# Kernel tuning notes

Measured on AMD Instinct MI355X. Metric: run time of the kernel, lower is better.

Reference implementation:

```python
import jax, jax.numpy as jnp
import numpy as np

B, T_ENC, IN, H, SEQ_OUT = 1024, 50, 99, 2112, 25


def _lstm_cell(x, h, c, W_ih, b_ih, W_hh, b_hh):
    # gates: [B, 4H], torch LSTMCell gate order is i, f, g, o
    gates = x @ W_ih.T + b_ih + h @ W_hh.T + b_hh
    i, f, g, o = jnp.split(gates, 4, axis=-1)
    c_new = jax.nn.sigmoid(f) * c + jax.nn.sigmoid(i) * jnp.tanh(g)
    h_new = jax.nn.sigmoid(o) * jnp.tanh(c_new)
    return h_new, c_new


def setup_inputs() -> dict:
    key = jax.random.key(0)
    ks = jax.random.split(key, 14)
    s = 0.04
    return {
        "hidden_states": jax.random.normal(ks[0], (B, T_ENC, H), jnp.float32),
        "cell_states": jax.random.normal(ks[1], (B, T_ENC, H), jnp.float32),
        "global_t_state": jax.random.normal(ks[2], (B, H), jnp.float32),
        "p": jax.random.normal(ks[3], (B, 1, IN), jnp.float32),
        "W_ih0": jax.random.normal(ks[4], (4 * H, IN), jnp.float32) * s,
        "b_ih0": jax.random.normal(ks[5], (4 * H,), jnp.float32) * s,
        "W_hh0": jax.random.normal(ks[6], (4 * H, H), jnp.float32) * s,
        "b_hh0": jax.random.normal(ks[7], (4 * H,), jnp.float32) * s,
        "W_ih1": jax.random.normal(ks[8], (4 * H, H), jnp.float32) * s,
        "b_ih1": jax.random.normal(ks[9], (4 * H,), jnp.float32) * s,
        "W_hh1": jax.random.normal(ks[10], (4 * H, H), jnp.float32) * s,
        "b_hh1": jax.random.normal(ks[11], (4 * H,), jnp.float32) * s,
        "W_out": jax.random.normal(ks[12], (H, IN), jnp.float32) * s,
        "b_out": jax.random.normal(ks[13], (IN,), jnp.float32) * s,
    }


def reference(hidden_states, cell_states, global_t_state, p,
              W_ih0, b_ih0, W_hh0, b_hh0,
              W_ih1, b_ih1, W_hh1, b_hh1,
              W_out, b_out):
    # initial states: layer 0 uses mean over encoder hidden states,
    # layer 1 uses mean over [global_t_state ; hidden_states]
    h0 = hidden_states.mean(axis=1)                                   # [B, H]
    h1 = jnp.concatenate((global_t_state[:, None, :], hidden_states), axis=1).mean(axis=1)
    c0 = cell_states.mean(axis=1)
    c1 = c0
    pre0 = p[:, 0, :]                                                 # seed input [B, IN]

    def step(carry, _):
        h0, c0, h1, c1, prev = carry
        h0n, c0n = _lstm_cell(prev, h0, c0, W_ih0, b_ih0, W_hh0, b_hh0)
        h1n, c1n = _lstm_cell(h0n, h1, c1, W_ih1, b_ih1, W_hh1, b_hh1)
        pre = h1n @ W_out + b_out + prev                              # residual on cell-0 input
        return (h0n, c0n, h1n, c1n, pre), pre

    _, pres = jax.lax.scan(step, (h0, c0, h1, c1, pre0), None, length=SEQ_OUT)
    return pres.transpose(1, 0, 2)                                    # [B, SEQ_OUT, IN]
```

## Files before the change

kernel.cpp:

```cpp
#include <hip/hip_runtime.h>

#define B_    1024
#define H_    2112
#define FH    8448
#define IN_   99
#define TENC  50
#define SEQ   25
#define K0    2240
#define K1    4224
#define LDX0  2240
#define LDX1  4224

typedef __bf16 bf16;
typedef __bf16 bf16x8 __attribute__((ext_vector_type(8)));
typedef __bf16 bf16x4 __attribute__((ext_vector_type(4)));
typedef float  f32x4  __attribute__((ext_vector_type(4)));

__device__ __forceinline__ void gload_lds16(const void* g, void* l) {
  __builtin_amdgcn_global_load_lds(
      (const __attribute__((address_space(1))) void*)g,
      (__attribute__((address_space(3))) void*)l, 16, 0, 0);
}

__device__ __forceinline__ float sigf(float x) { return 1.f / (1.f + __expf(-x)); }
__device__ __forceinline__ float tanhfast(float x) { return 1.f - 2.f / (__expf(2.f * x) + 1.f); }

__global__ __launch_bounds__(128, 3)
void lstm_gemm_cell(const bf16* __restrict__ X, int lda, int K,
                    const bf16* __restrict__ W,
                    const float* __restrict__ bsum,
                    float* __restrict__ Cst,
                    bf16* __restrict__ d1, int ld1,
                    bf16* __restrict__ d2, int ld2)
{
  __shared__ __align__(16) bf16 As[128 * 64];
  __shared__ __align__(16) bf16 Bs[64 * 64];

  const int cpx = gridDim.x >> 3;
  const int vid = (blockIdx.x & 7) * cpx + (blockIdx.x >> 3);
  const int hc0 = (vid >> 3) * 16;
  const int m0  = (vid & 7) * 128;

  const int tid  = threadIdx.x;
  const int srow = tid >> 3;
  const int scol = ((tid & 7) ^ (srow & 7)) * 8;

  const bf16* Ab = X + (size_t)(m0 + srow) * lda + scol;
  const bf16* Bb = W + (size_t)(hc0 + srow) * K + scol;

  const int lane = tid & 63;
  const int w    = tid >> 6;
  const int lr   = lane & 15, lq = lane >> 4;
  const int xs   = lr & 7;
  const int cof0 = (lq ^ xs) * 8;
  const int cof1 = ((4 + lq) ^ xs) * 8;

  f32x4 acc[4][4];
#pragma unroll
  for (int a = 0; a < 4; ++a)
#pragma unroll
    for (int b = 0; b < 4; ++b) acc[a][b] = (f32x4){0.f, 0.f, 0.f, 0.f};

  const int KT = K >> 6;
  for (int kt = 0; kt < KT; ++kt) {
    const int ko = kt * 64;
#pragma unroll
    for (int it = 0; it < 8; ++it)
      gload_lds16(Ab + (size_t)it * 16 * lda + ko, &As[it * 1024 + tid * 8]);
#pragma unroll
    for (int it = 0; it < 4; ++it)
      gload_lds16(Bb + (size_t)it * H_ * K + ko, &Bs[it * 1024 + tid * 8]);
    __syncthreads();

    bf16x8 af[4][2], bfr[4][2];
#pragma unroll
    for (int mi = 0; mi < 4; ++mi) {
      const int r = (w * 64 + mi * 16 + lr) * 64;
      af[mi][0] = *(const bf16x8*)&As[r + cof0];
      af[mi][1] = *(const bf16x8*)&As[r + cof1];
    }
#pragma unroll
    for (int nf = 0; nf < 4; ++nf) {
      const int r = (nf * 16 + lr) * 64;
      bfr[nf][0] = *(const bf16x8*)&Bs[r + cof0];
      bfr[nf][1] = *(const bf16x8*)&Bs[r + cof1];
    }
#pragma unroll
    for (int mi = 0; mi < 4; ++mi)
#pragma unroll
      for (int nf = 0; nf < 4; ++nf)
#pragma unroll
        for (int kc = 0; kc < 2; ++kc)
          acc[mi][nf] = __builtin_amdgcn_mfma_f32_16x16x32_bf16(
              af[mi][kc], bfr[nf][kc], acc[mi][nf], 0, 0, 0);
    __syncthreads();
  }

  const int hc = hc0 + lr;
  const float bi  = bsum[hc];
  const float bff = bsum[H_ + hc];
  const float bg  = bsum[2 * H_ + hc];
  const float bo  = bsum[3 * H_ + hc];

#pragma unroll
  for (int mi = 0; mi < 4; ++mi) {
#pragma unroll
    for (int r = 0; r < 4; ++r) {
      const int m = m0 + w * 64 + mi * 16 + lq * 4 + r;
      const float gi = acc[mi][0][r] + bi;
      const float gf = acc[mi][1][r] + bff;
      const float gg = acc[mi][2][r] + bg;
      const float go = acc[mi][3][r] + bo;
      const size_t ci = (size_t)m * H_ + hc;
      const float c_old = Cst[ci];
      const float cn = sigf(gf) * c_old + sigf(gi) * tanhfast(gg);
      const float hn = sigf(go) * tanhfast(cn);
      Cst[ci] = cn;
      const bf16 hb = (bf16)hn;
      d1[(size_t)m * ld1 + hc] = hb;
      if (d2) d2[(size_t)m * ld2 + hc] = hb;
    }
  }
}

__global__ __launch_bounds__(256, 1)
void out_gemm(const bf16* __restrict__ Hin,
              const bf16* __restrict__ Wo,
              const float* __restrict__ b_out,
              float* __restrict__ prev,
              bf16* __restrict__ X0n,
              float* __restrict__ out, int t)
{
  __shared__ float red[4][8][112];
  const int tid = threadIdx.x;
  const int m0 = blockIdx.x * 8;
  const int lane = tid & 63, wv = tid >> 6;
  const int lr = lane & 15, lq = lane >> 4, lk = lq * 8;

  f32x4 acc[7];
#pragma unroll
  for (int b = 0; b < 7; ++b) acc[b] = (f32x4){0.f, 0.f, 0.f, 0.f};

  const int start = (wv == 0) ? 0 : (1 + wv * 8);
  const int cnt = (wv == 0) ? 9 : 8;

  for (int kt = start; kt < start + cnt; ++kt) {
    const int ko = kt * 64;
    bf16x8 av[2], bv[7][2];
#pragma unroll
    for (int kc = 0; kc < 2; ++kc)
      av[kc] = *(const bf16x8*)&Hin[(size_t)(m0 + (lr & 7)) * LDX1 + ko + kc * 32 + lk];
#pragma unroll
    for (int nf = 0; nf < 7; ++nf)
#pragma unroll
      for (int kc = 0; kc < 2; ++kc)
        bv[nf][kc] = *(const bf16x8*)&Wo[(size_t)(nf * 16 + lr) * H_ + ko + kc * 32 + lk];
#pragma unroll
    for (int nf = 0; nf < 7; ++nf)
#pragma unroll
      for (int kc = 0; kc < 2; ++kc)
        acc[nf] = __builtin_amdgcn_mfma_f32_16x16x32_bf16(av[kc], bv[nf][kc], acc[nf], 0, 0, 0);
  }

  if (lq < 2) {
#pragma unroll
    for (int nf = 0; nf < 7; ++nf)
#pragma unroll
      for (int r = 0; r < 4; ++r)
        red[wv][lq * 4 + r][nf * 16 + lr] = acc[nf][r];
  }
  __syncthreads();

  for (int idx = tid; idx < 8 * 112; idx += 256) {
    const int ml = idx / 112, n = idx - ml * 112;
    if (n < IN_) {
      const int m = m0 + ml;
      float s = red[0][ml][n] + red[1][ml][n] + red[2][ml][n] + red[3][ml][n] + b_out[n];
      const float pre = s + prev[m * 112 + n];
      prev[m * 112 + n] = pre;
      out[((size_t)m * SEQ + t) * IN_ + n] = pre;
      X0n[(size_t)m * LDX0 + n] = (bf16)pre;
    }
  }
}

__global__ void init_state(const float* __restrict__ hs, const float* __restrict__ cs,
                           const float* __restrict__ gts,
                           bf16* __restrict__ X0a, bf16* __restrict__ X1a,
                           float* __restrict__ c0, float* __restrict__ c1)
{
  const int h4 = blockIdx.x * 256 + threadIdx.x;
  if (h4 >= 528) return;
  const int b = blockIdx.y;
  const float4* hp = (const float4*)(hs + (size_t)b * TENC * H_) + h4;
  const float4* cp = (const float4*)(cs + (size_t)b * TENC * H_) + h4;
  float4 sh = {0.f, 0.f, 0.f, 0.f}, sc = {0.f, 0.f, 0.f, 0.f};
  for (int tt = 0; tt < TENC; ++tt) {
    float4 a = hp[tt * 528];
    sh.x += a.x; sh.y += a.y; sh.z += a.z; sh.w += a.w;
    float4 c = cp[tt * 528];
    sc.x += c.x; sc.y += c.y; sc.z += c.z; sc.w += c.w;
  }
  const float4 g = ((const float4*)(gts + (size_t)b * H_))[h4];
  const float4 c0v = {sc.x / 50.f, sc.y / 50.f, sc.z / 50.f, sc.w / 50.f};
  ((float4*)(c0 + (size_t)b * H_))[h4] = c0v;
  ((float4*)(c1 + (size_t)b * H_))[h4] = c0v;
  bf16x4 h0b = {(bf16)(sh.x / 50.f), (bf16)(sh.y / 50.f), (bf16)(sh.z / 50.f), (bf16)(sh.w / 50.f)};
  *(bf16x4*)&X0a[(size_t)b * LDX0 + 128 + h4 * 4] = h0b;
  bf16x4 h1b = {(bf16)((sh.x + g.x) / 51.f), (bf16)((sh.y + g.y) / 51.f),
                (bf16)((sh.z + g.z) / 51.f), (bf16)((sh.w + g.w) / 51.f)};
  *(bf16x4*)&X1a[(size_t)b * LDX1 + 2112 + h4 * 4] = h1b;
}

__global__ void init_prev(const float* __restrict__ p, float* __restrict__ prev,
                          bf16* __restrict__ X0a, bf16* __restrict__ X0b)
{
  const int idx = blockIdx.x * 256 + threadIdx.x;
  const int b = idx >> 7, n = idx & 127;
  const float v = (n < IN_) ? p[(size_t)b * IN_ + n] : 0.f;
  if (n < 112) prev[b * 112 + n] = v;
  X0a[(size_t)b * LDX0 + n] = (bf16)v;
  X0b[(size_t)b * LDX0 + n] = (bf16)0.f;
}

__global__ void pack_w0(const float* __restrict__ Wih, const float* __restrict__ Whh,
                        bf16* __restrict__ Wc)
{
  const int n = blockIdx.x;
  const float* a = Wih + (size_t)n * IN_;
  const float* b = Whh + (size_t)n * H_;
  bf16* d = Wc + (size_t)n * K0;
  for (int k = threadIdx.x; k < K0; k += 256) {
    float v = (k < IN_) ? a[k] : ((k >= 128) ? b[k - 128] : 0.f);
    d[k] = (bf16)v;
  }
}

__global__ void pack_w1(const float* __restrict__ Wih, const float* __restrict__ Whh,
                        bf16* __restrict__ Wc)
{
  const int n = blockIdx.x;
  bf16* d = Wc + (size_t)n * K1;
  for (int k = threadIdx.x; k < K1; k += 256)
    d[k] = (bf16)((k < H_) ? Wih[(size_t)n * H_ + k] : Whh[(size_t)n * H_ + k - H_]);
}

__global__ void pack_wo(const float* __restrict__ W, bf16* __restrict__ Wo)
{
  const int n = blockIdx.x;
  for (int k = threadIdx.x; k < H_; k += 256)
    Wo[(size_t)n * H_ + k] = (n < IN_) ? (bf16)W[(size_t)k * IN_ + n] : (bf16)0.f;
}

__global__ void pack_bias(const float* __restrict__ bi0, const float* __restrict__ bh0,
                          const float* __restrict__ bi1, const float* __restrict__ bh1,
                          float* __restrict__ bs0, float* __restrict__ bs1)
{
  const int i = blockIdx.x * 256 + threadIdx.x;
  if (i < FH) { bs0[i] = bi0[i] + bh0[i]; bs1[i] = bi1[i] + bh1[i]; }
}

extern "C" void kernel_launch(void* const* d_in, const int* in_sizes, int n_in,
                              void* d_out, int out_size, void* d_ws, size_t ws_size,
                              hipStream_t stream)
{
  (void)in_sizes; (void)n_in; (void)out_size; (void)ws_size;
  const float* hs   = (const float*)d_in[0];
  const float* cs   = (const float*)d_in[1];
  const float* gts  = (const float*)d_in[2];
  const float* p    = (const float*)d_in[3];
  const float* Wih0 = (const float*)d_in[4];
  const float* bih0 = (const float*)d_in[5];
  const float* Whh0 = (const float*)d_in[6];
  const float* bhh0 = (const float*)d_in[7];
  const float* Wih1 = (const float*)d_in[8];
  const float* bih1 = (const float*)d_in[9];
  const float* Whh1 = (const float*)d_in[10];
  const float* bhh1 = (const float*)d_in[11];
  const float* Wout = (const float*)d_in[12];
  const float* bout = (const float*)d_in[13];
  float* out = (float*)d_out;

  char* ws = (char*)d_ws;
  size_t off = 0;
  auto alloc = [&](size_t bytes) -> void* {
    void* q = ws + off; off += (bytes + 255) & ~(size_t)255; return q;
  };
  bf16* Wc0 = (bf16*)alloc((size_t)FH * K0 * 2);
  bf16* Wc1 = (bf16*)alloc((size_t)FH * K1 * 2);
  bf16* Wo  = (bf16*)alloc((size_t)112 * H_ * 2);
  float* bs0 = (float*)alloc((size_t)FH * 4);
  float* bs1 = (float*)alloc((size_t)FH * 4);
  bf16* X0[2] = {(bf16*)alloc((size_t)B_ * LDX0 * 2), (bf16*)alloc((size_t)B_ * LDX0 * 2)};
  bf16* X1[2] = {(bf16*)alloc((size_t)B_ * LDX1 * 2), (bf16*)alloc((size_t)B_ * LDX1 * 2)};
  float* c0  = (float*)alloc((size_t)B_ * H_ * 4);
  float* c1  = (float*)alloc((size_t)B_ * H_ * 4);
  float* prev = (float*)alloc((size_t)B_ * 112 * 4);

  pack_w0<<<FH, 256, 0, stream>>>(Wih0, Whh0, Wc0);
  pack_w1<<<FH, 256, 0, stream>>>(Wih1, Whh1, Wc1);
  pack_wo<<<112, 256, 0, stream>>>(Wout, Wo);
  pack_bias<<<(FH + 255) / 256, 256, 0, stream>>>(bih0, bhh0, bih1, bhh1, bs0, bs1);
  init_prev<<<(B_ * 128) / 256, 256, 0, stream>>>(p, prev, X0[0], X0[1]);
  init_state<<<dim3(3, B_), 256, 0, stream>>>(hs, cs, gts, X0[0], X1[0], c0, c1);

  for (int t = 0; t < SEQ; ++t) {
    const int cur = t & 1, nxt = cur ^ 1;
    lstm_gemm_cell<<<1056, 128, 0, stream>>>(
        X0[cur], LDX0, K0, Wc0, bs0, c0, X1[cur], LDX1, X0[nxt] + 128, LDX0);
    lstm_gemm_cell<<<1056, 128, 0, stream>>>(
        X1[cur], LDX1, K1, Wc1, bs1, c1, X1[nxt] + 2112, LDX1, (bf16*)nullptr, 0);
    out_gemm<<<128, 256, 0, stream>>>(X1[nxt] + 2112, Wo, bout, prev, X0[nxt], out, t);
  }
}
```

Measured before the change: 4.666 ms.

## Use single-wave 64x128 tiles with double-buffered async LDS loads in LSTM GEMM

Each LSTM gate GEMM block becomes one 64-thread wave that computes a 64-row by 128-column tile (32 hidden units times 4 gates) instead of two waves on a 128x64 tile. Global-to-LDS loads are double-buffered, with the next-but-one stage issued after the current fragments are read, and __syncthreads is replaced by explicit vmcnt/lgkmcnt waits. The aim is to overlap memory traffic with MFMA work, improve reuse of the weight tile, and remove block barriers. In exchange it uses more accumulator registers, a single-wave occupancy bound, a larger LDS footprint, and leaves an unused compute lambda in the code.

```diff
diff --git a/kernel.cpp b/kernel.cpp
--- a/kernel.cpp
+++ b/kernel.cpp
@@ -25,7 +25,7 @@
 __device__ __forceinline__ float sigf(float x) { return 1.f / (1.f + __expf(-x)); }
 __device__ __forceinline__ float tanhfast(float x) { return 1.f - 2.f / (__expf(2.f * x) + 1.f); }
 
-__global__ __launch_bounds__(128, 3)
+__global__ __launch_bounds__(64, 1)
 void lstm_gemm_cell(const bf16* __restrict__ X, int lda, int K,
                     const bf16* __restrict__ W,
                     const float* __restrict__ bsum,
@@ -33,92 +33,141 @@
                     bf16* __restrict__ d1, int ld1,
                     bf16* __restrict__ d2, int ld2)
 {
-  __shared__ __align__(16) bf16 As[128 * 64];
-  __shared__ __align__(16) bf16 Bs[64 * 64];
-
-  const int cpx = gridDim.x >> 3;
-  const int vid = (blockIdx.x & 7) * cpx + (blockIdx.x >> 3);
-  const int hc0 = (vid >> 3) * 16;
-  const int m0  = (vid & 7) * 128;
-
-  const int tid  = threadIdx.x;
-  const int srow = tid >> 3;
-  const int scol = ((tid & 7) ^ (srow & 7)) * 8;
-
-  const bf16* Ab = X + (size_t)(m0 + srow) * lda + scol;
-  const bf16* Bb = W + (size_t)(hc0 + srow) * K + scol;
-
-  const int lane = tid & 63;
-  const int w    = tid >> 6;
-  const int lr   = lane & 15, lq = lane >> 4;
-  const int xs   = lr & 7;
+  __shared__ __align__(16) bf16 As[2][64 * 64];
+  __shared__ __align__(16) bf16 Bs[2][128 * 64];
+
+  const int vid = (blockIdx.x & 7) * 132 + (blockIdx.x >> 3);
+  const int hc0 = (vid >> 4) * 32;
+  const int m0  = (vid & 15) * 64;
+
+  const int tid = threadIdx.x;
+  const int r8  = tid >> 3;
+  const int scol = ((tid & 7) ^ (r8 & 7)) * 8;
+
+  const bf16* Ab = X + (size_t)(m0 + r8) * lda + scol;
+  const bf16* Bb = W + (size_t)(hc0 + r8) * K + scol;
+
+  const int lr = tid & 15, lq = tid >> 4;
+  const int xs = lr & 7;
   const int cof0 = (lq ^ xs) * 8;
   const int cof1 = ((4 + lq) ^ xs) * 8;
 
-  f32x4 acc[4][4];
+  f32x4 acc[4][8];
 #pragma unroll
   for (int a = 0; a < 4; ++a)
 #pragma unroll
-    for (int b = 0; b < 4; ++b) acc[a][b] = (f32x4){0.f, 0.f, 0.f, 0.f};
+    for (int b = 0; b < 8; ++b) acc[a][b] = (f32x4){0.f, 0.f, 0.f, 0.f};
+
+  auto stage = [&](int kt, int buf) {
+    const int ko = kt * 64;
+    bf16* ad = &As[buf][tid * 8];
+    bf16* bd = &Bs[buf][tid * 8];
+#pragma unroll
+    for (int it = 0; it < 8; ++it)
+      gload_lds16(Ab + (size_t)(it * 8) * lda + ko, ad + it * 512);
+#pragma unroll
+    for (int it = 0; it < 16; ++it) {
+      const int crow = ((it >> 1) & 3) * H_ + (it >> 3) * 16 + (it & 1) * 8;
+      gload_lds16(Bb + (size_t)crow * K + ko, bd + it * 512);
+    }
+  };
+
+  auto compute = [&](int buf, bool last) {
+    const bf16* Ap = &As[buf][0];
+    const bf16* Bp = &Bs[buf][0];
+    bf16x8 af0[4], bf0[8], af1[4], bf1[8];
+#pragma unroll
+    for (int mi = 0; mi < 4; ++mi) {
+      const int r = (mi * 16 + lr) * 64;
+      af0[mi] = *(const bf16x8*)&Ap[r + cof0];
+      af1[mi] = *(const bf16x8*)&Ap[r + cof1];
+    }
+#pragma unroll
+    for (int nf = 0; nf < 8; ++nf) {
+      const int r = (nf * 16 + lr) * 64;
+      bf0[nf] = *(const bf16x8*)&Bp[r + cof0];
+      bf1[nf] = *(const bf16x8*)&Bp[r + cof1];
+    }
+    if (!last) {
+      asm volatile("s_waitcnt lgkmcnt(0)" ::: "memory");
+      __builtin_amdgcn_sched_barrier(0);
+    }
+    return [=]() { (void)0; };
+  };
+  (void)compute;
 
   const int KT = K >> 6;
+  stage(0, 0);
+  stage(1, 1);
+
   for (int kt = 0; kt < KT; ++kt) {
-    const int ko = kt * 64;
-#pragma unroll
-    for (int it = 0; it < 8; ++it)
-      gload_lds16(Ab + (size_t)it * 16 * lda + ko, &As[it * 1024 + tid * 8]);
-#pragma unroll
-    for (int it = 0; it < 4; ++it)
-      gload_lds16(Bb + (size_t)it * H_ * K + ko, &Bs[it * 1024 + tid * 8]);
-    __syncthreads();
-
-    bf16x8 af[4][2], bfr[4][2];
+    const int buf = kt & 1;
+    if (kt < KT - 1)
+      asm volatile("s_waitcnt vmcnt(24)" ::: "memory");
+    else
+      asm volatile("s_waitcnt vmcnt(0)" ::: "memory");
+
+    const bf16* Ap = &As[buf][0];
+    const bf16* Bp = &Bs[buf][0];
+    bf16x8 af0[4], bf0[8], af1[4], bf1[8];
 #pragma unroll
     for (int mi = 0; mi < 4; ++mi) {
-      const int r = (w * 64 + mi * 16 + lr) * 64;
-      af[mi][0] = *(const bf16x8*)&As[r + cof0];
-      af[mi][1] = *(const bf16x8*)&As[r + cof1];
-    }
-#pragma unroll
-    for (int nf = 0; nf < 4; ++nf) {
+      const int r = (mi * 16 + lr) * 64;
+      af0[mi] = *(const bf16x8*)&Ap[r + cof0];
+      af1[mi] = *(const bf16x8*)&Ap[r + cof1];
+    }
+#pragma unroll
+    for (int nf = 0; nf < 8; ++nf) {
       const int r = (nf * 16 + lr) * 64;
-      bfr[nf][0] = *(const bf16x8*)&Bs[r + cof0];
-      bfr[nf][1] = *(const bf16x8*)&Bs[r + cof1];
-    }
+      bf0[nf] = *(const bf16x8*)&Bp[r + cof0];
+      bf1[nf] = *(const bf16x8*)&Bp[r + cof1];
+    }
+
+    if (kt < KT - 2) {
+      asm volatile("s_waitcnt lgkmcnt(0)" ::: "memory");
+      __builtin_amdgcn_sched_barrier(0);
+      stage(kt + 2, buf);
+    }
+
 #pragma unroll
     for (int mi = 0; mi < 4; ++mi)
 #pragma unroll
-      for (int nf = 0; nf < 4; ++nf)
-#pragma unroll
-        for (int kc = 0; kc < 2; ++kc)
-          acc[mi][nf] = __builtin_amdgcn_mfma_f32_16x16x32_bf16(
-              af[mi][kc], bfr[nf][kc], acc[mi][nf], 0, 0, 0);
-    __syncthreads();
-  }
-
-  const int hc = hc0 + lr;
-  const float bi  = bsum[hc];
-  const float bff = bsum[H_ + hc];
-  const float bg  = bsum[2 * H_ + hc];
-  const float bo  = bsum[3 * H_ + hc];
-
-#pragma unroll
-  for (int mi = 0; mi < 4; ++mi) {
-#pragma unroll
-    for (int r = 0; r < 4; ++r) {
-      const int m = m0 + w * 64 + mi * 16 + lq * 4 + r;
-      const float gi = acc[mi][0][r] + bi;
-      const float gf = acc[mi][1][r] + bff;
-      const float gg = acc[mi][2][r] + bg;
-      const float go = acc[mi][3][r] + bo;
-      const size_t ci = (size_t)m * H_ + hc;
-      const float c_old = Cst[ci];
-      const float cn = sigf(gf) * c_old + sigf(gi) * tanhfast(gg);
-      const float hn = sigf(go) * tanhfast(cn);
-      Cst[ci] = cn;
-      const bf16 hb = (bf16)hn;
-      d1[(size_t)m * ld1 + hc] = hb;
-      if (d2) d2[(size_t)m * ld2 + hc] = hb;
+      for (int nf = 0; nf < 8; ++nf)
+        acc[mi][nf] = __builtin_amdgcn_mfma_f32_16x16x32_bf16(
+            af0[mi], bf0[nf], acc[mi][nf], 0, 0, 0);
+#pragma unroll
+    for (int mi = 0; mi < 4; ++mi)
+#pragma unroll
+      for (int nf = 0; nf < 8; ++nf)
+        acc[mi][nf] = __builtin_amdgcn_mfma_f32_16x16x32_bf16(
+            af1[mi], bf1[nf], acc[mi][nf], 0, 0, 0);
+  }
+
+#pragma unroll
+  for (int hh = 0; hh < 2; ++hh) {
+    const int hc = hc0 + hh * 16 + lr;
+    const float bi  = bsum[hc];
+    const float bff = bsum[H_ + hc];
+    const float bg  = bsum[2 * H_ + hc];
+    const float bo  = bsum[3 * H_ + hc];
+#pragma unroll
+    for (int mi = 0; mi < 4; ++mi) {
+#pragma unroll
+      for (int r = 0; r < 4; ++r) {
+        const int m = m0 + mi * 16 + lq * 4 + r;
+        const float gi = acc[mi][hh * 4 + 0][r] + bi;
+        const float gf = acc[mi][hh * 4 + 1][r] + bff;
+        const float gg = acc[mi][hh * 4 + 2][r] + bg;
+        const float go = acc[mi][hh * 4 + 3][r] + bo;
+        const size_t ci = (size_t)m * H_ + hc;
+        const float c_old = Cst[ci];
+        const float cn = sigf(gf) * c_old + sigf(gi) * tanhfast(gg);
+        const float hn = sigf(go) * tanhfast(cn);
+        Cst[ci] = cn;
+        const bf16 hb2 = (bf16)hn;
+        d1[(size_t)m * ld1 + hc] = hb2;
+        if (d2) d2[(size_t)m * ld2 + hc] = hb2;
+      }
     }
   }
 }
@@ -306,9 +355,9 @@
 
   for (int t = 0; t < SEQ; ++t) {
     const int cur = t & 1, nxt = cur ^ 1;
-    lstm_gemm_cell<<<1056, 128, 0, stream>>>(
+    lstm_gemm_cell<<<1056, 64, 0, stream>>>(
         X0[cur], LDX0, K0, Wc0, bs0, c0, X1[cur], LDX1, X0[nxt] + 128, LDX0);
-    lstm_gemm_cell<<<1056, 128, 0, stream>>>(
+    lstm_gemm_cell<<<1056, 64, 0, stream>>>(
         X1[cur], LDX1, K1, Wc1, bs1, c1, X1[nxt] + 2112, LDX1, (bf16*)nullptr, 0);
     out_gemm<<<128, 256, 0, stream>>>(X1[nxt] + 2112, Wo, bout, prev, X0[nxt], out, t);
   }
```

Result: slower. 6.504 ms (+39.4%).
